# Performance work log

Hardware: AMD Instinct MI355X
Metric: run time of the kernel (lower is better)

## Reference

```python
import jax, jax.numpy as jnp
import numpy as np

DIM = 1024
NUM_HEADS = 8  # only used for the scale; heads are never actually split
SCALE = float((DIM // NUM_HEADS) ** 0.5)


def _attn(x, wq, wk, wv):
    # Single-head full-dim attention, faithful to the source (no head split).
    Q = x @ wq.T  # [B,S,D]
    K = x @ wk.T
    V = x @ wv.T
    scores = jnp.einsum('bqd,bkd->bqk', Q, K) / SCALE  # [B,S,S]
    attn = jax.nn.softmax(scores, axis=-1)
    return jnp.einsum('bqk,bkd->bqd', attn, V)


def setup_inputs() -> dict:
    key = jax.random.key(0)
    ks = jax.random.split(key, 9)
    B, S, D = 4, 2048, DIM
    w = lambda k: jax.random.normal(k, (D, D), dtype=jnp.float32) * 0.02
    return {
        'x': jax.random.normal(ks[0], (B, S, D), dtype=jnp.float32),
        'wq1': w(ks[1]), 'wk1': w(ks[2]), 'wv1': w(ks[3]),
        'fc1_w': w(ks[4]),
        'wq2': w(ks[5]), 'wk2': w(ks[6]), 'wv2': w(ks[7]),
        'fc2_w': w(ks[8]),
    }


def reference(x, wq1, wk1, wv1, fc1_w, wq2, wk2, wv2, fc2_w):
    h = _attn(x, wq1, wk1, wv1)
    h = jax.nn.silu(h)
    h = h @ fc1_w.T
    h = _attn(h, wq2, wk2, wv2)
    h = jax.nn.silu(h)
    h = h @ fc2_w.T
    return jax.nn.softmax(h, axis=-1)
```

## Files before the change

### kernel.cpp

```cpp
#include <hip/hip_runtime.h>
#include <math.h>


typedef __attribute__((ext_vector_type(8))) int i32x8;
typedef __attribute__((ext_vector_type(4))) int i32x4;
typedef __attribute__((ext_vector_type(4))) float f32x4;
typedef unsigned char u8;
typedef unsigned int u32;

#define EPI_F8 1
#define EPI_RV 2
#define EPI_EXP 3
#define EPI_PV 4
#define EPI_EXPF32 5

__device__ __forceinline__ void gload_lds16(const void* g, void* l) {
    __builtin_amdgcn_global_load_lds(
        (const __attribute__((address_space(1))) void*)g,
        (__attribute__((address_space(3))) void*)l, 16, 0, 0);
}

__device__ __forceinline__ u8 cvt_f8(float v) {
    return (u8)(__builtin_amdgcn_cvt_pk_fp8_f32(v, v, 0, false) & 0xFF);
}

__device__ __forceinline__ u32 pack_f8x4(float v0, float v1, float v2, float v3) {
    int p01 = __builtin_amdgcn_cvt_pk_fp8_f32(v0, v1, 0, false);
    int p23 = __builtin_amdgcn_cvt_pk_fp8_f32(v2, v3, 0, false);
    return (u32)(p01 & 0xFFFF) | ((u32)p23 << 16);
}

template <int EPI>
__global__ __launch_bounds__(256) void gemm_fp8(
    const u8* __restrict__ A, const u8* __restrict__ B,
    void* __restrict__ C0, void* __restrict__ C1, void* __restrict__ C2,
    int K, int ldA, int ldB, int ldC,
    long long bsA, long long bsB, long long bsC, float alpha, float beta)
{
    __shared__ u8 sA[128 * 128];
    __shared__ u8 sB[128 * 128];

    const int tid = threadIdx.x;
    const int wave = tid >> 6, lane = tid & 63;
    const int wm = wave >> 1, wn = wave & 1;
    const int m0 = blockIdx.y * 128, n0 = blockIdx.x * 128;
    const long long z = blockIdx.z;

    const u8* pA = A + z * bsA;
    const u8* pB = B + z * bsB;

    int blkid[4], rs_[4], cs16[4];
#pragma unroll
    for (int i = 0; i < 4; i++) {
        blkid[i] = wave * 256 + i * 64 + lane;
        rs_[i] = blkid[i] >> 3;
        cs16[i] = ((blkid[i] & 7) ^ (rs_[i] & 7)) * 16;
    }

    f32x4 acc[4][4] = {};
    const int fr = lane & 15, fc2 = (lane >> 4) * 2;

    for (int k0 = 0; k0 < K; k0 += 128) {
#pragma unroll
        for (int i = 0; i < 4; i++) {
            gload_lds16(pA + (long long)(m0 + rs_[i]) * ldA + k0 + cs16[i],
                        sA + blkid[i] * 16);
            gload_lds16(pB + (long long)(n0 + rs_[i]) * ldB + k0 + cs16[i],
                        sB + blkid[i] * 16);
        }
        __syncthreads();

        i32x8 a[4], b[4];
#pragma unroll
        for (int i = 0; i < 4; i++) {
            const int row = wm * 64 + i * 16 + fr;
            const int sw = row & 7;
            i32x4 lo = *(const i32x4*)(sA + row * 128 + ((fc2 + 0) ^ sw) * 16);
            i32x4 hi = *(const i32x4*)(sA + row * 128 + ((fc2 + 1) ^ sw) * 16);
            a[i] = __builtin_shufflevector(lo, hi, 0, 1, 2, 3, 4, 5, 6, 7);
        }
#pragma unroll
        for (int j = 0; j < 4; j++) {
            const int row = wn * 64 + j * 16 + fr;
            const int sw = row & 7;
            i32x4 lo = *(const i32x4*)(sB + row * 128 + ((fc2 + 0) ^ sw) * 16);
            i32x4 hi = *(const i32x4*)(sB + row * 128 + ((fc2 + 1) ^ sw) * 16);
            b[j] = __builtin_shufflevector(lo, hi, 0, 1, 2, 3, 4, 5, 6, 7);
        }
#pragma unroll
        for (int i = 0; i < 4; i++)
#pragma unroll
            for (int j = 0; j < 4; j++)
                acc[i][j] = __builtin_amdgcn_mfma_scale_f32_16x16x128_f8f6f4(
                    a[i], b[j], acc[i][j], 0 , 0 ,
                    0, 0x7F7F7F7F, 0, 0x7F7F7F7F);
        __syncthreads();
    }

    const int col = lane & 15;
    const int rbase = (lane >> 4) * 4;

    if (EPI == EPI_EXP) {
        u8* P = (u8*)C0 + z * bsC;
        float* rsum = (float*)C1 + z * 2048;
#pragma unroll
        for (int j = 0; j < 4; j++) {
            const int Cq = n0 + wn * 64 + j * 16 + col;
            float part = 0.f;
#pragma unroll
            for (int i = 0; i < 4; i++) {
                const int R0 = m0 + wm * 64 + i * 16 + rbase;
                float e0 = __expf(acc[i][j][0] * alpha);
                float e1 = __expf(acc[i][j][1] * alpha);
                float e2 = __expf(acc[i][j][2] * alpha);
                float e3 = __expf(acc[i][j][3] * alpha);
                part += (e0 + e1) + (e2 + e3);
                *(u32*)(P + (long long)Cq * ldC + R0) =
                    pack_f8x4(e0 * 0.0625f, e1 * 0.0625f,
                              e2 * 0.0625f, e3 * 0.0625f);
            }
            part += __shfl_xor(part, 16);
            part += __shfl_xor(part, 32);
            if (lane < 16) atomicAdd(&rsum[Cq], part);
        }
        return;
    }

    if (EPI == EPI_EXPF32) {
        float* Cw = (float*)C0;
        float* rsum = (float*)C1;
#pragma unroll
        for (int j = 0; j < 4; j++) {
            const int Cq = n0 + wn * 64 + j * 16 + col;
            float part = 0.f;
#pragma unroll
            for (int i = 0; i < 4; i++) {
                const int R0 = m0 + wm * 64 + i * 16 + rbase;
                float4 e;
                e.x = __expf(acc[i][j][0] * alpha);
                e.y = __expf(acc[i][j][1] * alpha);
                e.z = __expf(acc[i][j][2] * alpha);
                e.w = __expf(acc[i][j][3] * alpha);
                part += (e.x + e.y) + (e.z + e.w);
                *(float4*)(Cw + (long long)Cq * ldC + R0) = e;
            }
            part += __shfl_xor(part, 16);
            part += __shfl_xor(part, 32);
            if (lane < 16) atomicAdd(&rsum[Cq], part);
        }
        return;
    }

#pragma unroll
    for (int j = 0; j < 4; j++) {
        const int Cq = n0 + wn * 64 + j * 16 + col;
        float inv;
        if (EPI == EPI_PV) {
            const float* rsum = (const float*)C1 + z * 2048;
            inv = alpha / rsum[Cq];
        }
#pragma unroll
        for (int i = 0; i < 4; i++) {
            const int R0 = m0 + wm * 64 + i * 16 + rbase;
            if (EPI == EPI_F8) {
                u8* C = (u8*)C0 + z * bsC;
                *(u32*)(C + (long long)Cq * ldC + R0) =
                    pack_f8x4(acc[i][j][0] * alpha, acc[i][j][1] * alpha,
                              acc[i][j][2] * alpha, acc[i][j][3] * alpha);
            } else if (EPI == EPI_PV) {
                u8* C = (u8*)C0 + z * bsC;
                float v[4];
#pragma unroll
                for (int r = 0; r < 4; r++) {
                    float t = acc[i][j][r] * inv;
                    v[r] = (t / (1.f + __expf(-t))) * beta;
                }
                *(u32*)(C + (long long)Cq * ldC + R0) =
                    pack_f8x4(v[0], v[1], v[2], v[3]);
            } else {
                const int seg = R0 >> 10;
                const int db = R0 & 1023;
                if (seg == 1) {
                    const int bb = Cq >> 11, tt = Cq & 2047;
                    u8* VTp = (u8*)C2;
#pragma unroll
                    for (int r = 0; r < 4; r++)
                        VTp[(long long)bb * (1024LL * 2048) +
                            (long long)(db + r) * 2048 + tt] =
                            cvt_f8(acc[i][j][r] * beta);
                } else {
                    u8* C = (u8*)C0;
                    *(u32*)(C + (long long)Cq * 1024 + db) =
                        pack_f8x4(acc[i][j][0] * alpha, acc[i][j][1] * alpha,
                                  acc[i][j][2] * alpha, acc[i][j][3] * alpha);
                }
            }
        }
    }
}

__global__ __launch_bounds__(256) void convert_all(
    const float* x, const float* wv1, const float* wv2, const float* fc1,
    const float* fc2, u8* __restrict__ ax, u8* __restrict__ bproj,
    u8* __restrict__ wfc, float* __restrict__ rz)
{
    const int bid = blockIdx.x;
    if (bid < 24) {
        float4 zero = {0.f, 0.f, 0.f, 0.f};
        *(float4*)(rz + ((long long)bid * 256 + threadIdx.x) * 4) = zero;
    }
    const float* src;
    u8* dst;
    float scale;
    long long i;
    if (bid < 8192) {
        src = x; dst = ax; scale = 8.f;
        i = ((long long)bid * 256 + threadIdx.x) * 4;
    } else {
        const int idx = bid - 8192;
        const int wi = idx >> 10;
        const float* srcs[4] = {wv1, wv2, fc1, fc2};
        u8* dsts[4] = {bproj + (1 << 20), bproj + 3 * (1 << 20),
                       wfc, wfc + (1 << 20)};
        src = srcs[wi]; dst = dsts[wi]; scale = 256.f;
        i = (((long long)(idx & 1023)) * 256 + threadIdx.x) * 4;
    }
    float4 v = *(const float4*)(src + i);
    *(u32*)(dst + i) = pack_f8x4(v.x * scale, v.y * scale,
                                 v.z * scale, v.w * scale);
}

__global__ __launch_bounds__(256) void convert_t(
    const float* wq1, const float* wk1, const float* wq2, const float* wk2,
    u8* __restrict__ o)
{
    const float* srcs[4] = {wq1, wk1, wq2, wk2};
    const float* src = srcs[blockIdx.y];
    u8* dst = o + (long long)blockIdx.y * (1 << 20);
    const int q0 = (blockIdx.x & 15) * 64, d0 = (blockIdx.x >> 4) * 64;
    const int qq = (threadIdx.x & 15) * 4, dd = (threadIdx.x >> 4) * 4;
    float4 v[4];
#pragma unroll
    for (int s = 0; s < 4; s++)
        v[s] = *(const float4*)(src + (long long)(q0 + qq + s) * 1024 + d0 + dd);
    const float* vf = (const float*)v;
#pragma unroll
    for (int r = 0; r < 4; r++)
        *(u32*)(dst + (long long)(d0 + dd + r) * 1024 + q0 + qq) =
            pack_f8x4(vf[0 * 4 + r] * 256.f, vf[1 * 4 + r] * 256.f,
                      vf[2 * 4 + r] * 256.f, vf[3 * 4 + r] * 256.f);
}

__global__ __launch_bounds__(256) void normalize_1024(
    const float* __restrict__ e, const float* __restrict__ rsum,
    float* __restrict__ out)
{
    const long long row = blockIdx.x;
    const float inv = 1.0f / rsum[row];
    const float* p = e + row * 1024;
    float* o = out + row * 1024;
    float4 v = *(const float4*)(p + threadIdx.x * 4);
    float4 ov;
    ov.x = v.x * inv; ov.y = v.y * inv; ov.z = v.z * inv; ov.w = v.w * inv;
    *(float4*)(o + threadIdx.x * 4) = ov;
}

extern "C" void kernel_launch(void* const* d_in, const int* in_sizes, int n_in,
                              void* d_out, int out_size, void* d_ws, size_t ws_size,
                              hipStream_t stream)
{
    float* out = (float*)d_out;

    constexpr int Bt = 4, S = 2048, D = 1024;
    constexpr int M = Bt * S;
    const long long MD = (long long)M * D;
    const long long DD = (long long)D * D;
    const long long SD = (long long)S * D;
    const long long SS = (long long)S * S;

    u8* Af = (u8*)d_ws;
    u8* Bproj = Af + MD;
    u8* WqT = Bproj + 2 * 2048 * 1024;
    u8* Wfc = WqT + 4 * DD;
    u8* Rf = Wfc + 2 * DD;
    u8* VT = Rf + MD;
    u8* Pf = VT + MD;
    u8* Hs = Pf + (long long)Bt * SS;
    float* SC = (float*)(Hs + MD);
    float* rsum0 = SC + MD;
    float* rsum1 = rsum0 + M;
    float* rsum2 = rsum1 + M;

    const dim3 blk(256);

    const float SOFT = 0.08838834764831845f;
    const float a_d1   = 1.f / 64.f;
    const float a_R[2] = {1.f / 512.f, 1.f / 1024.f};
    const float b_V[2] = {1.f / 256.f, 1.f / 64.f};
    const float a_qk[2] = {SOFT / 128.f, SOFT / 65536.f};
    const float a_pv[2] = {2.0f, 1.f / 64.f};
    const float b_pv[2] = {256.f, 65536.f};
    const float a_fc[2] = {256.f / 65536.f, 1.f / 16777216.f};

    convert_all<<<dim3(12288), blk, 0, stream>>>(
        (const float*)d_in[0], (const float*)d_in[3], (const float*)d_in[7],
        (const float*)d_in[4], (const float*)d_in[8], Af, Bproj, Wfc, rsum0);
    convert_t<<<dim3(256, 4), blk, 0, stream>>>(
        (const float*)d_in[1], (const float*)d_in[2], (const float*)d_in[5],
        (const float*)d_in[6], WqT);
    gemm_fp8<EPI_F8><<<dim3(8, 8, 2), blk, 0, stream>>>(
        WqT, WqT + DD, Bproj, nullptr, nullptr, D, D, D, D,
        2 * DD, 2 * DD, (long long)2048 * 1024, a_d1, 0.f);

    const dim3 grv(M / 128, 2048 / 128, 1);
    const dim3 gqk(S / 128, S / 128, Bt);
    const dim3 gpv(S / 128, D / 128, Bt);
    const dim3 gw(M / 128, D / 128, 1);

    for (int layer = 0; layer < 2; layer++) {
        const u8* bp = Bproj + (long long)layer * 2048 * 1024;
        const u8* fc = Wfc + (long long)layer * DD;
        float* rsum = layer ? rsum1 : rsum0;

        gemm_fp8<EPI_RV><<<grv, blk, 0, stream>>>(
            bp, Af, Rf, nullptr, VT, D, D, D, D, 0, 0, 0,
            a_R[layer], b_V[layer]);
        gemm_fp8<EPI_EXP><<<gqk, blk, 0, stream>>>(
            Af, Rf, Pf, rsum, nullptr, D, D, D, S, SD, SD, SS,
            a_qk[layer], 0.f);
        gemm_fp8<EPI_PV><<<gpv, blk, 0, stream>>>(
            VT, Pf, Hs, rsum, nullptr, S, S, S, D,
            (long long)D * S, SS, SD, a_pv[layer], b_pv[layer]);
        if (layer == 0) {
            gemm_fp8<EPI_F8><<<gw, blk, 0, stream>>>(
                fc, Hs, Af, nullptr, nullptr, D, D, D, D, 0, 0, 0,
                a_fc[0], 0.f);
        } else {
            gemm_fp8<EPI_EXPF32><<<gw, blk, 0, stream>>>(
                fc, Hs, SC, rsum2, nullptr, D, D, D, D, 0, 0, 0,
                a_fc[1], 0.f);
        }
    }

    normalize_1024<<<dim3(M), blk, 0, stream>>>(SC, rsum2, out);
}
```

Before: 334.7 us.

## Add 128x256-tile 8-wave FP8 GEMM with triple-buffered LDS pipeline

Adds a gemm256 kernel that uses 512 threads, a 128x256 output tile and three LDS buffers. Global-to-LDS loads are issued two stages ahead and waited on with explicit vmcnt, and MFMA priority is raised during compute. The per-layer GEMMs now use it with halved grid x dimension. The old gemm_fp8 keeps only the F8 epilogue for the initial weight projection. The aim is to hide memory latency and raise B-tile reuse, at the cost of much more LDS per block (144KB), which lowers occupancy and leaves fewer blocks to fill the grid.

```diff
diff --git a/kernel.cpp b/kernel.cpp
--- a/kernel.cpp
+++ b/kernel.cpp
@@ -96,6 +96,128 @@
                     0, 0x7F7F7F7F, 0, 0x7F7F7F7F);
         __syncthreads();
     }
+
+    const int col = lane & 15;
+    const int rbase = (lane >> 4) * 4;
+
+    if (EPI == EPI_F8) {
+#pragma unroll
+        for (int j = 0; j < 4; j++) {
+            const int Cq = n0 + wn * 64 + j * 16 + col;
+#pragma unroll
+            for (int i = 0; i < 4; i++) {
+                const int R0 = m0 + wm * 64 + i * 16 + rbase;
+                u8* C = (u8*)C0 + z * bsC;
+                *(u32*)(C + (long long)Cq * ldC + R0) =
+                    pack_f8x4(acc[i][j][0] * alpha, acc[i][j][1] * alpha,
+                              acc[i][j][2] * alpha, acc[i][j][3] * alpha);
+            }
+        }
+    }
+    (void)beta; (void)C1; (void)C2;
+}
+
+template <int EPI>
+__global__ __launch_bounds__(512, 2) void gemm256(
+    const u8* __restrict__ A, const u8* __restrict__ B,
+    void* __restrict__ C0, void* __restrict__ C1, void* __restrict__ C2,
+    int K, int ldA, int ldB, int ldC,
+    long long bsA, long long bsB, long long bsC, float alpha, float beta)
+{
+    __shared__ __align__(16) u8 sA[3][128 * 128];
+    __shared__ __align__(16) u8 sB[3][256 * 128];
+
+    const int tid = threadIdx.x;
+    const int wave = tid >> 6, lane = tid & 63;
+    const int wm = wave >> 2, wn = wave & 3;
+    const int m0 = blockIdx.y * 128, n0 = blockIdx.x * 256;
+    const long long z = blockIdx.z;
+
+    const u8* pA = A + z * bsA;
+    const u8* pB = B + z * bsB;
+
+    long long offA[2], offB[4];
+    int dstA[2], dstB[4];
+#pragma unroll
+    for (int l = 0; l < 2; l++) {
+        const int id = l * 512 + tid;
+        const int r = id >> 3, c = (id & 7) ^ (r & 7);
+        offA[l] = (long long)(m0 + r) * ldA + c * 16;
+        dstA[l] = id * 16;
+    }
+#pragma unroll
+    for (int l = 0; l < 4; l++) {
+        const int id = l * 512 + tid;
+        const int r = id >> 3, c = (id & 7) ^ (r & 7);
+        offB[l] = (long long)(n0 + r) * ldB + c * 16;
+        dstB[l] = id * 16;
+    }
+
+    f32x4 acc[4][4] = {};
+    const int fr = lane & 15, fc2 = (lane >> 4) * 2;
+    const int NT = K >> 7;
+
+    auto STAGE = [&](int t, int buf) {
+        const long long kb = (long long)t << 7;
+#pragma unroll
+        for (int l = 0; l < 2; l++)
+            gload_lds16(pA + offA[l] + kb, &sA[buf][dstA[l]]);
+#pragma unroll
+        for (int l = 0; l < 4; l++)
+            gload_lds16(pB + offB[l] + kb, &sB[buf][dstB[l]]);
+    };
+
+    auto COMPUTE = [&](int buf) {
+        i32x8 a[4], b[4];
+#pragma unroll
+        for (int i = 0; i < 4; i++) {
+            const int row = wm * 64 + i * 16 + fr;
+            const int sw = row & 7;
+            const u8* p = &sA[buf][row * 128];
+            i32x4 lo = *(const i32x4*)(p + ((fc2 + 0) ^ sw) * 16);
+            i32x4 hi = *(const i32x4*)(p + ((fc2 + 1) ^ sw) * 16);
+            a[i] = __builtin_shufflevector(lo, hi, 0, 1, 2, 3, 4, 5, 6, 7);
+        }
+#pragma unroll
+        for (int j = 0; j < 4; j++) {
+            const int row = wn * 64 + j * 16 + fr;
+            const int sw = row & 7;
+            const u8* p = &sB[buf][row * 128];
+            i32x4 lo = *(const i32x4*)(p + ((fc2 + 0) ^ sw) * 16);
+            i32x4 hi = *(const i32x4*)(p + ((fc2 + 1) ^ sw) * 16);
+            b[j] = __builtin_shufflevector(lo, hi, 0, 1, 2, 3, 4, 5, 6, 7);
+        }
+        __builtin_amdgcn_s_setprio(1);
+#pragma unroll
+        for (int i = 0; i < 4; i++)
+#pragma unroll
+            for (int j = 0; j < 4; j++)
+                acc[i][j] = __builtin_amdgcn_mfma_scale_f32_16x16x128_f8f6f4(
+                    a[i], b[j], acc[i][j], 0 , 0 ,
+                    0, 0x7F7F7F7F, 0, 0x7F7F7F7F);
+        __builtin_amdgcn_s_setprio(0);
+    };
+
+    STAGE(0, 0);
+    STAGE(1, 1);
+    asm volatile("s_waitcnt vmcnt(6)" ::: "memory");
+    __builtin_amdgcn_s_barrier();
+    __builtin_amdgcn_sched_barrier(0);
+
+    int c0 = 0, c1 = 1, c2 = 2;
+    for (int t = 0; t < NT - 2; ++t) {
+        STAGE(t + 2, c2);
+        COMPUTE(c0);
+        asm volatile("s_waitcnt vmcnt(6) lgkmcnt(0)" ::: "memory");
+        __builtin_amdgcn_s_barrier();
+        __builtin_amdgcn_sched_barrier(0);
+        const int tmp = c0; c0 = c1; c1 = c2; c2 = tmp;
+    }
+    COMPUTE(c0);
+    asm volatile("s_waitcnt vmcnt(0) lgkmcnt(0)" ::: "memory");
+    __builtin_amdgcn_s_barrier();
+    __builtin_amdgcn_sched_barrier(0);
+    COMPUTE(c1);
 
     const int col = lane & 15;
     const int rbase = (lane >> 4) * 4;
@@ -292,6 +414,7 @@
     float* rsum2 = rsum1 + M;
 
     const dim3 blk(256);
+    const dim3 blk2(512);
 
     const float SOFT = 0.08838834764831845f;
     const float a_d1   = 1.f / 64.f;
@@ -312,31 +435,31 @@
         WqT, WqT + DD, Bproj, nullptr, nullptr, D, D, D, D,
         2 * DD, 2 * DD, (long long)2048 * 1024, a_d1, 0.f);
 
-    const dim3 grv(M / 128, 2048 / 128, 1);
-    const dim3 gqk(S / 128, S / 128, Bt);
-    const dim3 gpv(S / 128, D / 128, Bt);
-    const dim3 gw(M / 128, D / 128, 1);
+    const dim3 grv(M / 256, 2048 / 128, 1);
+    const dim3 gqk(S / 256, S / 128, Bt);
+    const dim3 gpv(S / 256, D / 128, Bt);
+    const dim3 gw(M / 256, D / 128, 1);
 
     for (int layer = 0; layer < 2; layer++) {
         const u8* bp = Bproj + (long long)layer * 2048 * 1024;
         const u8* fc = Wfc + (long long)layer * DD;
         float* rsum = layer ? rsum1 : rsum0;
 
-        gemm_fp8<EPI_RV><<<grv, blk, 0, stream>>>(
+        gemm256<EPI_RV><<<grv, blk2, 0, stream>>>(
             bp, Af, Rf, nullptr, VT, D, D, D, D, 0, 0, 0,
             a_R[layer], b_V[layer]);
-        gemm_fp8<EPI_EXP><<<gqk, blk, 0, stream>>>(
+        gemm256<EPI_EXP><<<gqk, blk2, 0, stream>>>(
             Af, Rf, Pf, rsum, nullptr, D, D, D, S, SD, SD, SS,
             a_qk[layer], 0.f);
-        gemm_fp8<EPI_PV><<<gpv, blk, 0, stream>>>(
+        gemm256<EPI_PV><<<gpv, blk2, 0, stream>>>(
             VT, Pf, Hs, rsum, nullptr, S, S, S, D,
             (long long)D * S, SS, SD, a_pv[layer], b_pv[layer]);
         if (layer == 0) {
-            gemm_fp8<EPI_F8><<<gw, blk, 0, stream>>>(
+            gemm256<EPI_F8><<<gw, blk2, 0, stream>>>(
                 fc, Hs, Af, nullptr, nullptr, D, D, D, D, 0, 0, 0,
                 a_fc[0], 0.f);
         } else {
-            gemm_fp8<EPI_EXPF32><<<gw, blk, 0, stream>>>(
+            gemm256<EPI_EXPF32><<<gw, blk2, 0, stream>>>(
                 fc, Hs, SC, rsum2, nullptr, D, D, D, D, 0, 0, 0,
                 a_fc[1], 0.f);
         }
```

New measurement: 357.4 us. 6.8% more time.
